# Performance work log

Measured on AMD Instinct MI355X. Metric: run time of the kernel, lower is better.

The kernel has to match this reference:

```python
import jax, jax.numpy as jnp
import numpy as np

N_NODES = 100000
N_EDGES = 1600000
DIM_IN = 128
DIM_OUT = 128


def setup_inputs() -> dict:
    key = jax.random.key(0)
    k_x, k_w, k_r, k_c, k_v = jax.random.split(key, 5)
    x = jax.random.normal(k_x, (N_NODES, DIM_IN), dtype=jnp.float32)
    # Linear(dim_in, dim_out, bias=False): weight is [dim_out, dim_in]
    W = jax.random.normal(k_w, (DIM_OUT, DIM_IN), dtype=jnp.float32) * (1.0 / np.sqrt(DIM_IN))
    edge_row = jax.random.randint(k_r, (N_EDGES,), 0, N_NODES, dtype=jnp.int32)
    edge_col = jax.random.randint(k_c, (N_EDGES,), 0, N_NODES, dtype=jnp.int32)
    edge_val = jax.random.uniform(k_v, (N_EDGES,), dtype=jnp.float32)
    return {"x": x, "W": W, "edge_row": edge_row, "edge_col": edge_col, "edge_val": edge_val}


def reference(x, W, edge_row, edge_col, edge_val):
    # h = x @ W.T   (Linear, no bias)  -> [N, dim_out]
    h = jnp.einsum('nd,od->no', x, W)
    # SpMM: out[i] = sum_{e: row[e]==i} val[e] * h[col[e]]
    msgs = edge_val[:, None] * h[edge_col]          # [E, dim_out] irregular gather
    out = jax.ops.segment_sum(msgs, edge_row, num_segments=N_NODES)  # scatter-add
    return out
```

## Files before the change

kernel.cpp:

```cpp
#include <hip/hip_runtime.h>

#define DIM 128
#define NBINS 196
#define RPBIN 512
#define BCAP 9216
#define BATCH 2048
#define NSORT 392
#define CPAD 16

typedef __bf16 bf16x8 __attribute__((ext_vector_type(8)));
typedef __bf16 bf16x2 __attribute__((ext_vector_type(2)));
typedef float  f32x4  __attribute__((ext_vector_type(4)));

__global__ __launch_bounds__(256) void prep(const float* __restrict__ W,
                                            __bf16* __restrict__ Wb,
                                            int* __restrict__ ccur) {
    int i = blockIdx.x * 256 + threadIdx.x;
    if (i < DIM * DIM) Wb[i] = (__bf16)W[i];
    int j = i - DIM * DIM;
    if (j >= 0 && j < NBINS * CPAD) ccur[j] = 0;
}

__global__ __launch_bounds__(256) void gemm_and_sort(
    const float* __restrict__ x, const __bf16* __restrict__ Wb,
    __bf16* __restrict__ hb, int n_nodes,
    const int* __restrict__ er, const int* __restrict__ ec,
    const float* __restrict__ ev, int* __restrict__ ccur,
    uint2* __restrict__ coarse, int n_edges, int n_gemm_blocks) {

    __shared__ int   bhist[NBINS];
    __shared__ int   boffs[NBINS];
    __shared__ int   gbase[NBINS];
    __shared__ uint2 sc8[BATCH];

    if ((int)blockIdx.x < n_gemm_blocks) {
        const int wave = threadIdx.x >> 6;
        const int lane = threadIdx.x & 63;
        const int m = lane & 15, q = lane >> 4;
        const int nodebase = blockIdx.x * 64 + wave * 16;
        int rowA = nodebase + m;
        if (rowA >= n_nodes) rowA = n_nodes - 1;

        f32x4 acc[8];
#pragma unroll
        for (int t = 0; t < 8; ++t) acc[t] = (f32x4){0.f, 0.f, 0.f, 0.f};

#pragma unroll
        for (int s = 0; s < 4; ++s) {
            const float* xp = x + (size_t)rowA * DIM + s * 32 + q * 8;
            float4 xa = *(const float4*)xp;
            float4 xb = *(const float4*)(xp + 4);
            bf16x8 a;
            a[0] = (__bf16)xa.x; a[1] = (__bf16)xa.y;
            a[2] = (__bf16)xa.z; a[3] = (__bf16)xa.w;
            a[4] = (__bf16)xb.x; a[5] = (__bf16)xb.y;
            a[6] = (__bf16)xb.z; a[7] = (__bf16)xb.w;
#pragma unroll
            for (int t = 0; t < 8; ++t) {
                bf16x8 b = *(const bf16x8*)(Wb + (size_t)(t * 16 + m) * DIM + s * 32 + q * 8);
                acc[t] = __builtin_amdgcn_mfma_f32_16x16x32_bf16(a, b, acc[t], 0, 0, 0);
            }
        }
#pragma unroll
        for (int reg = 0; reg < 4; ++reg) {
            int r = nodebase + q * 4 + reg;
            if (r < n_nodes) {
                __bf16* hp = hb + (size_t)r * DIM + m;
#pragma unroll
                for (int t = 0; t < 8; ++t)
                    hp[t * 16] = (__bf16)acc[t][reg];
            }
        }
        return;
    }

    const int wg  = blockIdx.x - n_gemm_blocks;
    const int tid = threadIdx.x;
    const int nbatch = (n_edges + BATCH - 1) / BATCH;

    for (int batch = wg; batch < nbatch; batch += NSORT) {
        const int b0 = batch * BATCH;

        for (int i = tid; i < NBINS; i += 256) bhist[i] = 0;
        __syncthreads();

        int      rows[8];
        unsigned lov[8];
        int      slot[8];
#pragma unroll
        for (int k = 0; k < 8; ++k) {
            int e = b0 + k * 256 + tid;
            if (e < n_edges) {
                int r = er[e], c = ec[e];
                float v = ev[e];
                unsigned q = (unsigned)(v * 32768.f + 0.5f);
                if (q > 32767u) q = 32767u;
                rows[k] = r;
                lov[k]  = (q << 17) | (unsigned)c;
                slot[k] = atomicAdd(&bhist[r >> 9], 1);
            } else rows[k] = -1;
        }
        __syncthreads();

        if (tid < NBINS) boffs[tid] = bhist[tid];
        __syncthreads();
        for (int d = 1; d < NBINS; d <<= 1) {
            int t = (tid < NBINS && tid >= d) ? boffs[tid - d] : 0;
            __syncthreads();
            if (tid < NBINS) boffs[tid] += t;
            __syncthreads();
        }
        if (tid < NBINS) boffs[tid] -= bhist[tid];
        __syncthreads();

        if (tid < NBINS) {
            int len = bhist[tid];
            gbase[tid] = len ? atomicAdd(&ccur[tid * CPAD], len) : 0;
        }

#pragma unroll
        for (int k = 0; k < 8; ++k) {
            if (rows[k] >= 0) {
                int bin = rows[k] >> 9;
                sc8[boffs[bin] + slot[k]] = make_uint2(lov[k], (unsigned)rows[k]);
            }
        }
        __syncthreads();

        const int total = boffs[NBINS - 1] + bhist[NBINS - 1];
        for (int j = tid; j < total; j += 256) {
            uint2 s = sc8[j];
            int bin = (int)(s.y >> 9);
            int pos = gbase[bin] + (j - boffs[bin]);
            if (pos < BCAP)
                coarse[(size_t)bin * BCAP + pos] = s;
        }
        __syncthreads();
    }
}

__global__ __launch_bounds__(512) void bin_sort(
    const uint2* __restrict__ coarse, const int* __restrict__ ccur,
    unsigned* __restrict__ fine, int* __restrict__ offs,
    int* __restrict__ cnt, int n_nodes) {

    __shared__ int      cntA[RPBIN];
    __shared__ int      base[RPBIN];
    __shared__ unsigned fsc[BCAP];

    const int bin = blockIdx.x;
    const int tid = threadIdx.x;
    int nb = ccur[bin * CPAD];
    if (nb > BCAP) nb = BCAP;
    const uint2* src = coarse + (size_t)bin * BCAP;

    cntA[tid] = 0;
    __syncthreads();
    for (int i = tid; i < nb; i += 512)
        atomicAdd(&cntA[src[i].y & (RPBIN - 1)], 1);
    __syncthreads();

    base[tid] = cntA[tid];
    __syncthreads();
    for (int d = 1; d < RPBIN; d <<= 1) {
        int t = (tid >= d) ? base[tid - d] : 0;
        __syncthreads();
        base[tid] += t;
        __syncthreads();
    }
    base[tid] -= cntA[tid];
    __syncthreads();

    {
        int r = bin * RPBIN + tid;
        if (r < n_nodes) {
            offs[r] = bin * BCAP + base[tid];
            cnt[r]  = cntA[tid];
        }
    }
    __syncthreads();

    for (int i = tid; i < nb; i += 512) {
        uint2 e = src[i];
        int s = atomicAdd(&base[e.y & (RPBIN - 1)], 1);
        fsc[s] = e.x;
    }
    __syncthreads();

    for (int i = tid; i < nb; i += 512)
        fine[(size_t)bin * BCAP + i] = fsc[i];
}

__global__ __launch_bounds__(256) void segment_reduce(
    const unsigned* __restrict__ fine, const int* __restrict__ offs,
    const int* __restrict__ cnt, const __bf16* __restrict__ hb,
    float* __restrict__ out, int n_nodes) {

    const int rs = threadIdx.x >> 6;
    const int f  = threadIdx.x & 63;
    const int r  = blockIdx.x * 4 + rs;
    __shared__ unsigned sp[4][64];

    const bool valid = r < n_nodes;
    const int n = valid ? cnt[r] : 0;
    const int o = valid ? offs[r] : 0;
    if (valid && f < n && f < 64) sp[rs][f] = fine[(size_t)o + f];
    __syncthreads();
    if (!valid) return;

    float2 acc = make_float2(0.f, 0.f);
#pragma unroll 4
    for (int j = 0; j < n; ++j) {
        unsigned p = (j < 64) ? sp[rs][j] : fine[(size_t)o + j];
        float v  = (float)(p >> 17) * (1.f / 32768.f);
        int col  = (int)(p & 0x1FFFFu);
        bf16x2 h2 = *(const bf16x2*)(hb + (size_t)col * DIM + 2 * f);
        acc.x += v * (float)h2[0];
        acc.y += v * (float)h2[1];
    }
    *(float2*)(out + (size_t)r * DIM + 2 * f) = acc;
}

extern "C" void kernel_launch(void* const* d_in, const int* in_sizes, int n_in,
                              void* d_out, int out_size, void* d_ws, size_t ws_size,
                              hipStream_t stream) {
    const float* x  = (const float*)d_in[0];
    const float* W  = (const float*)d_in[1];
    const int*   er = (const int*)d_in[2];
    const int*   ec = (const int*)d_in[3];
    const float* ev = (const float*)d_in[4];
    float* out = (float*)d_out;

    const int n_nodes = in_sizes[0] / DIM;
    const int n_edges = in_sizes[2];

    char* wsb = (char*)d_ws;
    __bf16* Wb   = (__bf16*)wsb;
    __bf16* hb   = (__bf16*)(wsb + 32768);
    uint2*  coarse = (uint2*)(wsb + 32768 + (size_t)n_nodes * DIM * 2);
    unsigned* fine = (unsigned*)((char*)coarse + (size_t)NBINS * BCAP * 8);
    int* ccur = (int*)((char*)fine + (size_t)NBINS * BCAP * 4);
    int* offs = ccur + NBINS * CPAD;
    int* cnt  = offs + n_nodes;

    prep<<<(DIM * DIM + NBINS * CPAD + 255) / 256, 256, 0, stream>>>(W, Wb, ccur);

    const int n_gemm_blocks = (n_nodes + 63) / 64;
    gemm_and_sort<<<n_gemm_blocks + NSORT, 256, 0, stream>>>(
        x, Wb, hb, n_nodes, er, ec, ev, ccur, coarse, n_edges, n_gemm_blocks);

    bin_sort<<<NBINS, 512, 0, stream>>>(coarse, ccur, fine, offs, cnt, n_nodes);

    segment_reduce<<<(n_nodes + 3) / 4, 256, 0, stream>>>(
        fine, offs, cnt, hb, out, n_nodes);
}
```

Baseline: 230.6 us.

## Slice h into 16-feature column planes and reduce per slice with finer bins

```diff
diff --git a/kernel.cpp b/kernel.cpp
--- a/kernel.cpp
+++ b/kernel.cpp
@@ -1,12 +1,13 @@
 #include <hip/hip_runtime.h>
 
 #define DIM 128
-#define NBINS 196
-#define RPBIN 512
-#define BCAP 9216
+#define NBINS 392
+#define RPBIN 256
+#define BCAP 4736
 #define BATCH 2048
 #define NSORT 392
 #define CPAD 16
+#define SLICEF 16
 
 typedef __bf16 bf16x8 __attribute__((ext_vector_type(8)));
 typedef __bf16 bf16x2 __attribute__((ext_vector_type(2)));
@@ -23,7 +24,7 @@
 
 __global__ __launch_bounds__(256) void gemm_and_sort(
     const float* __restrict__ x, const __bf16* __restrict__ Wb,
-    __bf16* __restrict__ hb, int n_nodes,
+    __bf16* __restrict__ hbs, int n_nodes,
     const int* __restrict__ er, const int* __restrict__ ec,
     const float* __restrict__ ev, int* __restrict__ ccur,
     uint2* __restrict__ coarse, int n_edges, int n_gemm_blocks) {
@@ -31,6 +32,7 @@
     __shared__ int   bhist[NBINS];
     __shared__ int   boffs[NBINS];
     __shared__ int   gbase[NBINS];
+    __shared__ int   psum[NBINS / 2];
     __shared__ uint2 sc8[BATCH];
 
     if ((int)blockIdx.x < n_gemm_blocks) {
@@ -65,10 +67,9 @@
         for (int reg = 0; reg < 4; ++reg) {
             int r = nodebase + q * 4 + reg;
             if (r < n_nodes) {
-                __bf16* hp = hb + (size_t)r * DIM + m;
 #pragma unroll
                 for (int t = 0; t < 8; ++t)
-                    hp[t * 16] = (__bf16)acc[t][reg];
+                    hbs[((size_t)t * n_nodes + r) * SLICEF + m] = (__bf16)acc[t][reg];
             }
         }
         return;
@@ -97,31 +98,35 @@
                 if (q > 32767u) q = 32767u;
                 rows[k] = r;
                 lov[k]  = (q << 17) | (unsigned)c;
-                slot[k] = atomicAdd(&bhist[r >> 9], 1);
+                slot[k] = atomicAdd(&bhist[r >> 8], 1);
             } else rows[k] = -1;
         }
         __syncthreads();
 
-        if (tid < NBINS) boffs[tid] = bhist[tid];
-        __syncthreads();
-        for (int d = 1; d < NBINS; d <<= 1) {
-            int t = (tid < NBINS && tid >= d) ? boffs[tid - d] : 0;
+        if (tid < NBINS / 2) psum[tid] = bhist[2 * tid] + bhist[2 * tid + 1];
+        __syncthreads();
+        for (int d = 1; d < NBINS / 2; d <<= 1) {
+            int t = (tid < NBINS / 2 && tid >= d) ? psum[tid - d] : 0;
             __syncthreads();
-            if (tid < NBINS) boffs[tid] += t;
+            if (tid < NBINS / 2) psum[tid] += t;
             __syncthreads();
         }
-        if (tid < NBINS) boffs[tid] -= bhist[tid];
-        __syncthreads();
-
-        if (tid < NBINS) {
-            int len = bhist[tid];
-            gbase[tid] = len ? atomicAdd(&ccur[tid * CPAD], len) : 0;
+        if (tid < NBINS / 2) {
+            int b = tid ? psum[tid - 1] : 0;
+            boffs[2 * tid]     = b;
+            boffs[2 * tid + 1] = b + bhist[2 * tid];
+        }
+        __syncthreads();
+
+        for (int i = tid; i < NBINS; i += 256) {
+            int len = bhist[i];
+            gbase[i] = len ? atomicAdd(&ccur[i * CPAD], len) : 0;
         }
 
 #pragma unroll
         for (int k = 0; k < 8; ++k) {
             if (rows[k] >= 0) {
-                int bin = rows[k] >> 9;
+                int bin = rows[k] >> 8;
                 sc8[boffs[bin] + slot[k]] = make_uint2(lov[k], (unsigned)rows[k]);
             }
         }
@@ -130,7 +135,7 @@
         const int total = boffs[NBINS - 1] + bhist[NBINS - 1];
         for (int j = tid; j < total; j += 256) {
             uint2 s = sc8[j];
-            int bin = (int)(s.y >> 9);
+            int bin = (int)(s.y >> 8);
             int pos = gbase[bin] + (j - boffs[bin]);
             if (pos < BCAP)
                 coarse[(size_t)bin * BCAP + pos] = s;
@@ -139,7 +144,7 @@
     }
 }
 
-__global__ __launch_bounds__(512) void bin_sort(
+__global__ __launch_bounds__(256) void bin_sort(
     const uint2* __restrict__ coarse, const int* __restrict__ ccur,
     unsigned* __restrict__ fine, int* __restrict__ offs,
     int* __restrict__ cnt, int n_nodes) {
@@ -156,7 +161,7 @@
 
     cntA[tid] = 0;
     __syncthreads();
-    for (int i = tid; i < nb; i += 512)
+    for (int i = tid; i < nb; i += 256)
         atomicAdd(&cntA[src[i].y & (RPBIN - 1)], 1);
     __syncthreads();
 
@@ -169,7 +174,6 @@
         __syncthreads();
     }
     base[tid] -= cntA[tid];
-    __syncthreads();
 
     {
         int r = bin * RPBIN + tid;
@@ -180,45 +184,47 @@
     }
     __syncthreads();
 
-    for (int i = tid; i < nb; i += 512) {
+    for (int i = tid; i < nb; i += 256) {
         uint2 e = src[i];
         int s = atomicAdd(&base[e.y & (RPBIN - 1)], 1);
         fsc[s] = e.x;
     }
     __syncthreads();
 
-    for (int i = tid; i < nb; i += 512)
+    for (int i = tid; i < nb; i += 256)
         fine[(size_t)bin * BCAP + i] = fsc[i];
 }
 
-__global__ __launch_bounds__(256) void segment_reduce(
+__global__ __launch_bounds__(256) void slice_reduce(
     const unsigned* __restrict__ fine, const int* __restrict__ offs,
-    const int* __restrict__ cnt, const __bf16* __restrict__ hb,
+    const int* __restrict__ cnt, const __bf16* __restrict__ hbs,
     float* __restrict__ out, int n_nodes) {
 
-    const int rs = threadIdx.x >> 6;
-    const int f  = threadIdx.x & 63;
-    const int r  = blockIdx.x * 4 + rs;
-    __shared__ unsigned sp[4][64];
+    const int s    = blockIdx.x & 7;
+    const int rg   = blockIdx.x >> 3;
+    const int wave = threadIdx.x >> 6;
+    const int lane = threadIdx.x & 63;
+    const int g    = lane >> 3;
+    const int f    = lane & 7;
+    const int r    = rg * 32 + wave * 8 + g;
 
     const bool valid = r < n_nodes;
     const int n = valid ? cnt[r] : 0;
     const int o = valid ? offs[r] : 0;
-    if (valid && f < n && f < 64) sp[rs][f] = fine[(size_t)o + f];
-    __syncthreads();
-    if (!valid) return;
+    const __bf16* hs = hbs + (size_t)s * n_nodes * SLICEF;
 
     float2 acc = make_float2(0.f, 0.f);
-#pragma unroll 4
-    for (int j = 0; j < n; ++j) {
-        unsigned p = (j < 64) ? sp[rs][j] : fine[(size_t)o + j];
+#pragma unroll 2
+    for (int e = 0; e < n; ++e) {
+        unsigned p = fine[(size_t)o + e];
         float v  = (float)(p >> 17) * (1.f / 32768.f);
         int col  = (int)(p & 0x1FFFFu);
-        bf16x2 h2 = *(const bf16x2*)(hb + (size_t)col * DIM + 2 * f);
+        bf16x2 h2 = *(const bf16x2*)(hs + (size_t)col * SLICEF + 2 * f);
         acc.x += v * (float)h2[0];
         acc.y += v * (float)h2[1];
     }
-    *(float2*)(out + (size_t)r * DIM + 2 * f) = acc;
+    if (valid)
+        *(float2*)(out + (size_t)r * DIM + s * SLICEF + 2 * f) = acc;
 }
 
 extern "C" void kernel_launch(void* const* d_in, const int* in_sizes, int n_in,
@@ -235,8 +241,8 @@
     const int n_edges = in_sizes[2];
 
     char* wsb = (char*)d_ws;
-    __bf16* Wb   = (__bf16*)wsb;
-    __bf16* hb   = (__bf16*)(wsb + 32768);
+    __bf16* Wb  = (__bf16*)wsb;
+    __bf16* hbs = (__bf16*)(wsb + 32768);
     uint2*  coarse = (uint2*)(wsb + 32768 + (size_t)n_nodes * DIM * 2);
     unsigned* fine = (unsigned*)((char*)coarse + (size_t)NBINS * BCAP * 8);
     int* ccur = (int*)((char*)fine + (size_t)NBINS * BCAP * 4);
@@ -247,10 +253,11 @@
 
     const int n_gemm_blocks = (n_nodes + 63) / 64;
     gemm_and_sort<<<n_gemm_blocks + NSORT, 256, 0, stream>>>(
-        x, Wb, hb, n_nodes, er, ec, ev, ccur, coarse, n_edges, n_gemm_blocks);
-
-    bin_sort<<<NBINS, 512, 0, stream>>>(coarse, ccur, fine, offs, cnt, n_nodes);
-
-    segment_reduce<<<(n_nodes + 3) / 4, 256, 0, stream>>>(
-        fine, offs, cnt, hb, out, n_nodes);
-}
+        x, Wb, hbs, n_nodes, er, ec, ev, ccur, coarse, n_edges, n_gemm_blocks);
+
+    bin_sort<<<NBINS, 256, 0, stream>>>(coarse, ccur, fine, offs, cnt, n_nodes);
+
+    const int nrg = (n_nodes + 31) / 32;
+    slice_reduce<<<8 * nrg, 256, 0, stream>>>(
+        fine, offs, cnt, hbs, out, n_nodes);
+}
```

New measurement: 281.3 us. 1.22x slower.

## Use finer bins and split each bin sort across four blocks

Applied to the files above, without the earlier changes.

```diff
diff --git a/kernel.cpp b/kernel.cpp
--- a/kernel.cpp
+++ b/kernel.cpp
@@ -1,9 +1,10 @@
 #include <hip/hip_runtime.h>
 
 #define DIM 128
-#define NBINS 196
-#define RPBIN 512
-#define BCAP 9216
+#define NBINS 392
+#define RPBIN 256
+#define BCAP 4608
+#define QCAP 1152
 #define BATCH 2048
 #define NSORT 392
 #define CPAD 16
@@ -31,6 +32,7 @@
     __shared__ int   bhist[NBINS];
     __shared__ int   boffs[NBINS];
     __shared__ int   gbase[NBINS];
+    __shared__ int   psum[NBINS / 2];
     __shared__ uint2 sc8[BATCH];
 
     if ((int)blockIdx.x < n_gemm_blocks) {
@@ -97,31 +99,35 @@
                 if (q > 32767u) q = 32767u;
                 rows[k] = r;
                 lov[k]  = (q << 17) | (unsigned)c;
-                slot[k] = atomicAdd(&bhist[r >> 9], 1);
+                slot[k] = atomicAdd(&bhist[r >> 8], 1);
             } else rows[k] = -1;
         }
         __syncthreads();
 
-        if (tid < NBINS) boffs[tid] = bhist[tid];
-        __syncthreads();
-        for (int d = 1; d < NBINS; d <<= 1) {
-            int t = (tid < NBINS && tid >= d) ? boffs[tid - d] : 0;
+        if (tid < NBINS / 2) psum[tid] = bhist[2 * tid] + bhist[2 * tid + 1];
+        __syncthreads();
+        for (int d = 1; d < NBINS / 2; d <<= 1) {
+            int t = (tid < NBINS / 2 && tid >= d) ? psum[tid - d] : 0;
             __syncthreads();
-            if (tid < NBINS) boffs[tid] += t;
+            if (tid < NBINS / 2) psum[tid] += t;
             __syncthreads();
         }
-        if (tid < NBINS) boffs[tid] -= bhist[tid];
-        __syncthreads();
-
-        if (tid < NBINS) {
-            int len = bhist[tid];
-            gbase[tid] = len ? atomicAdd(&ccur[tid * CPAD], len) : 0;
+        if (tid < NBINS / 2) {
+            int b = tid ? psum[tid - 1] : 0;
+            boffs[2 * tid]     = b;
+            boffs[2 * tid + 1] = b + bhist[2 * tid];
+        }
+        __syncthreads();
+
+        for (int i = tid; i < NBINS; i += 256) {
+            int len = bhist[i];
+            gbase[i] = len ? atomicAdd(&ccur[i * CPAD], len) : 0;
         }
 
 #pragma unroll
         for (int k = 0; k < 8; ++k) {
             if (rows[k] >= 0) {
-                int bin = rows[k] >> 9;
+                int bin = rows[k] >> 8;
                 sc8[boffs[bin] + slot[k]] = make_uint2(lov[k], (unsigned)rows[k]);
             }
         }
@@ -130,7 +136,7 @@
         const int total = boffs[NBINS - 1] + bhist[NBINS - 1];
         for (int j = tid; j < total; j += 256) {
             uint2 s = sc8[j];
-            int bin = (int)(s.y >> 9);
+            int bin = (int)(s.y >> 8);
             int pos = gbase[bin] + (j - boffs[bin]);
             if (pos < BCAP)
                 coarse[(size_t)bin * BCAP + pos] = s;
@@ -139,24 +145,26 @@
     }
 }
 
-__global__ __launch_bounds__(512) void bin_sort(
+__global__ __launch_bounds__(256) void bin_sort4(
     const uint2* __restrict__ coarse, const int* __restrict__ ccur,
-    unsigned* __restrict__ fine, int* __restrict__ offs,
-    int* __restrict__ cnt, int n_nodes) {
+    unsigned* __restrict__ fine, unsigned* __restrict__ meta, int n_nodes) {
 
     __shared__ int      cntA[RPBIN];
     __shared__ int      base[RPBIN];
-    __shared__ unsigned fsc[BCAP];
-
-    const int bin = blockIdx.x;
+    __shared__ unsigned fsc[QCAP];
+
+    const int bin = blockIdx.x >> 2;
+    const int q   = blockIdx.x & 3;
     const int tid = threadIdx.x;
     int nb = ccur[bin * CPAD];
     if (nb > BCAP) nb = BCAP;
-    const uint2* src = coarse + (size_t)bin * BCAP;
+    const int beg = (nb * q) >> 2;
+    const int len = ((nb * (q + 1)) >> 2) - beg;
+    const uint2* src = coarse + (size_t)bin * BCAP + beg;
 
     cntA[tid] = 0;
     __syncthreads();
-    for (int i = tid; i < nb; i += 512)
+    for (int i = tid; i < len; i += 256)
         atomicAdd(&cntA[src[i].y & (RPBIN - 1)], 1);
     __syncthreads();
 
@@ -169,32 +177,30 @@
         __syncthreads();
     }
     base[tid] -= cntA[tid];
-    __syncthreads();
 
     {
         int r = bin * RPBIN + tid;
-        if (r < n_nodes) {
-            offs[r] = bin * BCAP + base[tid];
-            cnt[r]  = cntA[tid];
-        }
-    }
-    __syncthreads();
-
-    for (int i = tid; i < nb; i += 512) {
+        if (r < n_nodes)
+            meta[(size_t)r * 4 + q] =
+                ((unsigned)(q * QCAP + base[tid]) << 12) | (unsigned)cntA[tid];
+    }
+    __syncthreads();
+
+    for (int i = tid; i < len; i += 256) {
         uint2 e = src[i];
         int s = atomicAdd(&base[e.y & (RPBIN - 1)], 1);
         fsc[s] = e.x;
     }
     __syncthreads();
 
-    for (int i = tid; i < nb; i += 512)
-        fine[(size_t)bin * BCAP + i] = fsc[i];
+    unsigned* dst = fine + (size_t)bin * BCAP + q * QCAP;
+    for (int i = tid; i < len; i += 256)
+        dst[i] = fsc[i];
 }
 
 __global__ __launch_bounds__(256) void segment_reduce(
-    const unsigned* __restrict__ fine, const int* __restrict__ offs,
-    const int* __restrict__ cnt, const __bf16* __restrict__ hb,
-    float* __restrict__ out, int n_nodes) {
+    const unsigned* __restrict__ fine, const unsigned* __restrict__ meta,
+    const __bf16* __restrict__ hb, float* __restrict__ out, int n_nodes) {
 
     const int rs = threadIdx.x >> 6;
     const int f  = threadIdx.x & 63;
@@ -202,16 +208,38 @@
     __shared__ unsigned sp[4][64];
 
     const bool valid = r < n_nodes;
-    const int n = valid ? cnt[r] : 0;
-    const int o = valid ? offs[r] : 0;
-    if (valid && f < n && f < 64) sp[rs][f] = fine[(size_t)o + f];
+    int n = 0, p1 = 0, p2 = 0, p3 = 0;
+    size_t o0 = 0, o1 = 0, o2 = 0, o3 = 0;
+    if (valid) {
+        uint4 m = *(const uint4*)(meta + (size_t)r * 4);
+        size_t bb = (size_t)(r >> 8) * BCAP;
+        int c0 = m.x & 0xFFFu, c1 = m.y & 0xFFFu, c2 = m.z & 0xFFFu, c3 = m.w & 0xFFFu;
+        o0 = bb + (m.x >> 12); o1 = bb + (m.y >> 12);
+        o2 = bb + (m.z >> 12); o3 = bb + (m.w >> 12);
+        p1 = c0; p2 = p1 + c1; p3 = p2 + c2; n = p3 + c3;
+    }
+    if (valid && f < n && f < 64) {
+        size_t pos = (f < p1) ? o0 + f
+                   : (f < p2) ? o1 + (f - p1)
+                   : (f < p3) ? o2 + (f - p2)
+                   :            o3 + (f - p3);
+        sp[rs][f] = fine[pos];
+    }
     __syncthreads();
     if (!valid) return;
 
     float2 acc = make_float2(0.f, 0.f);
 #pragma unroll 4
     for (int j = 0; j < n; ++j) {
-        unsigned p = (j < 64) ? sp[rs][j] : fine[(size_t)o + j];
+        unsigned p;
+        if (j < 64) p = sp[rs][j];
+        else {
+            size_t pos = (j < p1) ? o0 + j
+                       : (j < p2) ? o1 + (j - p1)
+                       : (j < p3) ? o2 + (j - p2)
+                       :            o3 + (j - p3);
+            p = fine[pos];
+        }
         float v  = (float)(p >> 17) * (1.f / 32768.f);
         int col  = (int)(p & 0x1FFFFu);
         bf16x2 h2 = *(const bf16x2*)(hb + (size_t)col * DIM + 2 * f);
@@ -235,13 +263,12 @@
     const int n_edges = in_sizes[2];
 
     char* wsb = (char*)d_ws;
-    __bf16* Wb   = (__bf16*)wsb;
-    __bf16* hb   = (__bf16*)(wsb + 32768);
+    __bf16* Wb  = (__bf16*)wsb;
+    __bf16* hb  = (__bf16*)(wsb + 32768);
     uint2*  coarse = (uint2*)(wsb + 32768 + (size_t)n_nodes * DIM * 2);
     unsigned* fine = (unsigned*)((char*)coarse + (size_t)NBINS * BCAP * 8);
     int* ccur = (int*)((char*)fine + (size_t)NBINS * BCAP * 4);
-    int* offs = ccur + NBINS * CPAD;
-    int* cnt  = offs + n_nodes;
+    unsigned* meta = (unsigned*)((char*)ccur + (size_t)NBINS * CPAD * 4);
 
     prep<<<(DIM * DIM + NBINS * CPAD + 255) / 256, 256, 0, stream>>>(W, Wb, ccur);
 
@@ -249,8 +276,8 @@
     gemm_and_sort<<<n_gemm_blocks + NSORT, 256, 0, stream>>>(
         x, Wb, hb, n_nodes, er, ec, ev, ccur, coarse, n_edges, n_gemm_blocks);
 
-    bin_sort<<<NBINS, 512, 0, stream>>>(coarse, ccur, fine, offs, cnt, n_nodes);
+    bin_sort4<<<NBINS * 4, 256, 0, stream>>>(coarse, ccur, fine, meta, n_nodes);
 
     segment_reduce<<<(n_nodes + 3) / 4, 256, 0, stream>>>(
-        fine, offs, cnt, hb, out, n_nodes);
-}
+        fine, meta, hb, out, n_nodes);
+}
```

Measured after the change: 267.6 us. 16.0% more time.
